# Performance work log

Measured on AMD Instinct MI355X. Metric: run time of the kernel, lower is better.

Reference implementation:

```python
import jax, jax.numpy as jnp
import numpy as np

N, E, B, D, L = 100000, 600000, 128, 128, 3
BOT = 64
EPS = 1e-5


def _forward(query_x, corpus_x, gin_eps, mlp_W1, mlp_b1, mlp_W2, mlp_b2, bn_gamma, bn_beta,
             pool_G1, pool_g1b, pool_G2, pool_g2b, pool_Wm,
             int_G1, int_g1b, int_G2, int_g2b, int_F1, int_f1b, int_F2, int_f2b,
             sc_G1, sc_g1b, sc_G2, sc_g2b, sc_F1, sc_f1b, sc_F2, sc_f2b,
             query_edge_index, query_graph_idx, corpus_edge_index, corpus_graph_idx, num_graphs):
    def gin(x, ei, l):
        # GINConv: sum of source-node features into targets, plus (1+eps)*self
        agg = jax.ops.segment_sum(x[ei[0]], ei[1], num_segments=x.shape[0])
        h = (1.0 + gin_eps[l]) * x + agg
        h = jax.nn.relu(h @ mlp_W1[l] + mlp_b1[l]) @ mlp_W2[l] + mlp_b2[l]
        mu = h.mean(axis=0)
        var = ((h - mu) ** 2).mean(axis=0)  # biased var (BatchNorm training mode)
        h = (h - mu) * jax.lax.rsqrt(var + EPS) * bn_gamma[l] + bn_beta[l]
        return jax.nn.relu(h)  # dropout p=0.0

    def pool(x, gidx, l):
        coef = jnp.tanh(jax.nn.relu(x @ pool_G1[l] + pool_g1b[l]) @ pool_G2[l] + pool_g2b[l])
        s = (coef + 1.0) * x
        sums = jax.ops.segment_sum(s, gidx, num_segments=num_graphs)
        cnt = jax.ops.segment_sum(jnp.ones((x.shape[0],), x.dtype), gidx, num_segments=num_graphs)
        mean = sums / cnt[:, None]
        gc = jnp.tanh(mean @ pool_Wm[l])  # [B, D]
        node_coef = jax.nn.sigmoid(jnp.sum(s * gc[gidx], axis=1))  # [N]
        return jax.ops.segment_sum(node_coef[:, None] * s, gidx, num_segments=num_graphs)

    def interact(q, c, l):
        comb = jnp.concatenate([q, c], axis=1)  # [B, 2D]
        coef = jax.nn.sigmoid(jax.nn.relu(comb @ int_G1[l] + int_g1b[l]) @ int_G2[l] + int_g2b[l])
        sc = (coef + 1.0) * comb
        return jax.nn.relu(jax.nn.relu(sc @ int_F1[l] + int_f1b[l]) @ int_F2[l] + int_f2b[l])

    qx, cx = query_x, corpus_x
    feats = []
    for l in range(gin_eps.shape[0]):
        qx = gin(qx, query_edge_index, l)
        cx = gin(cx, corpus_edge_index, l)
        feats.append(interact(pool(qx, query_graph_idx, l), pool(cx, corpus_graph_idx, l), l))
    f = jnp.concatenate(feats, axis=1)  # [B, sum(filters)//2]
    coef = jax.nn.sigmoid(jax.nn.relu(f @ sc_G1 + sc_g1b) @ sc_G2 + sc_g2b)
    sf = (coef + 1.0) * f
    return (jax.nn.relu(sf @ sc_F1 + sc_f1b) @ sc_F2 + sc_f2b).squeeze(-1)  # [B]


def setup_inputs() -> dict:
    key = jax.random.key(0)
    kit = iter(jax.random.split(key, 64))
    def nrm(shape, s=0.05):
        return jax.random.normal(next(kit), shape, jnp.float32) * s
    C, R, OUT, AGG, RG = 2 * D, (2 * D) // 4, D // 2, (3 * D) // 2, ((3 * D) // 2) // 4
    inp = {
        "query_x": nrm((N, D), 1.0),
        "query_edge_index": jax.random.randint(next(kit), (2, E), 0, N),
        "query_graph_idx": jnp.sort(jax.random.randint(next(kit), (N,), 0, B)),
        "corpus_x": nrm((N, D), 1.0),
        "corpus_edge_index": jax.random.randint(next(kit), (2, E), 0, N),
        "corpus_graph_idx": jnp.sort(jax.random.randint(next(kit), (N,), 0, B)),
        "num_graphs": B,
        "gin_eps": jnp.zeros((L,), jnp.float32),
        "mlp_W1": nrm((L, D, D)), "mlp_b1": jnp.zeros((L, D)),
        "mlp_W2": nrm((L, D, D)), "mlp_b2": jnp.zeros((L, D)),
        "bn_gamma": jnp.ones((L, D)), "bn_beta": jnp.zeros((L, D)),
        "pool_G1": nrm((L, D, D // 4)), "pool_g1b": jnp.zeros((L, D // 4)),
        "pool_G2": nrm((L, D // 4, D)), "pool_g2b": jnp.zeros((L, D)),
        "pool_Wm": nrm((L, D, D)),
        "int_G1": nrm((L, C, R)), "int_g1b": jnp.zeros((L, R)),
        "int_G2": nrm((L, R, C)), "int_g2b": jnp.zeros((L, C)),
        "int_F1": nrm((L, C, C)), "int_f1b": jnp.zeros((L, C)),
        "int_F2": nrm((L, C, OUT)), "int_f2b": jnp.zeros((L, OUT)),
        "sc_G1": nrm((AGG, RG)), "sc_g1b": jnp.zeros((RG,)),
        "sc_G2": nrm((RG, AGG)), "sc_g2b": jnp.zeros((AGG,)),
        "sc_F1": nrm((AGG, BOT)), "sc_f1b": jnp.zeros((BOT,)),
        "sc_F2": nrm((BOT, 1)), "sc_f2b": jnp.zeros((1,)),
    }
    return inp


def reference(query_x, query_edge_index, query_graph_idx, corpus_x, corpus_edge_index, corpus_graph_idx,
              num_graphs, gin_eps, mlp_W1, mlp_b1, mlp_W2, mlp_b2, bn_gamma, bn_beta,
              pool_G1, pool_g1b, pool_G2, pool_g2b, pool_Wm,
              int_G1, int_g1b, int_G2, int_g2b, int_F1, int_f1b, int_F2, int_f2b,
              sc_G1, sc_g1b, sc_G2, sc_g2b, sc_F1, sc_f1b, sc_F2, sc_f2b):
    return _forward(query_x, corpus_x, gin_eps, mlp_W1, mlp_b1, mlp_W2, mlp_b2, bn_gamma, bn_beta,
                    pool_G1, pool_g1b, pool_G2, pool_g2b, pool_Wm,
                    int_G1, int_g1b, int_G2, int_g2b, int_F1, int_f1b, int_F2, int_f2b,
                    sc_G1, sc_g1b, sc_G2, sc_g2b, sc_F1, sc_f1b, sc_F2, sc_f2b,
                    query_edge_index, query_graph_idx, corpus_edge_index, corpus_graph_idx, num_graphs)
```

## Files before the change

### kernel.cpp

```cpp
#include <hip/hip_runtime.h>
#include <hip/hip_bf16.h>

constexpr int NN  = 100000;
constexpr int NN2 = 200000;
constexpr int NE  = 600000;
constexpr int NB  = 128;
constexpr int D   = 128;
constexpr int NL  = 3;
constexpr int CAP = 48;
constexpr int MT_TOT = NN2 / 16;
constexpr int MT_Q   = NN / 16;

typedef __bf16 bf16x8 __attribute__((ext_vector_type(8)));
typedef float f32x4 __attribute__((ext_vector_type(4)));
typedef unsigned short us8 __attribute__((ext_vector_type(8)));

__device__ __forceinline__ float sigmoidf_(float x) { return 1.0f / (1.0f + __expf(-x)); }
__device__ __forceinline__ unsigned short f2b(float f) {
    __hip_bfloat16 h = __float2bfloat16(f);
    return __builtin_bit_cast(unsigned short, h);
}
__device__ __forceinline__ float b2f(unsigned short u) {
    __hip_bfloat16 h = __builtin_bit_cast(__hip_bfloat16, u);
    return __bfloat162float(h);
}
__device__ __forceinline__ bf16x8 ldfrag(const unsigned short* p) {
    return __builtin_bit_cast(bf16x8, *(const us8*)p);
}

__global__ __launch_bounds__(256) void k_csr_fill(const int* __restrict__ qei, const int* __restrict__ cei,
                                                  int* __restrict__ deg, int* __restrict__ bucket) {
    int e = blockIdx.x * 256 + threadIdx.x;
    int src, dst;
    if (e < NE) {
        src = qei[e]; dst = qei[NE + e];
    } else if (e < 2 * NE) {
        src = cei[e - NE] + NN; dst = cei[NE + (e - NE)] + NN;
    } else return;
    int pos = atomicAdd(&deg[dst], 1);
    if (pos < CAP) bucket[(size_t)dst * CAP + pos] = src;
}

__global__ __launch_bounds__(256) void k_cnt(const int* __restrict__ gq, const int* __restrict__ gc,
                                             float* __restrict__ cnt) {
    __shared__ float h[256];
    for (int i = threadIdx.x; i < 256; i += 256) h[i] = 0.f;
    __syncthreads();
    int total = gridDim.x * 256;
    int tid = blockIdx.x * 256 + threadIdx.x;
    int per = (NN2 + total - 1) / total;
    int r0 = tid * per, r1 = min(r0 + per, NN2);
    if (r0 < r1) {
        int cur = (r0 < NN) ? gq[r0] : 128 + gc[r0 - NN];
        float c = 0.f;
        for (int r = r0; r < r1; ++r) {
            int g = (r < NN) ? gq[r] : 128 + gc[r - NN];
            if (g != cur) { atomicAdd(&h[cur], c); c = 0.f; cur = g; }
            c += 1.f;
        }
        atomicAdd(&h[cur], c);
    }
    __syncthreads();
    for (int i = threadIdx.x; i < 256; i += 256)
        if (h[i] != 0.f) atomicAdd(&cnt[i], h[i]);
}

__global__ __launch_bounds__(256) void k_wprep_all(
    const float* mW1, const float* mW2, const float* pG1, const float* pG2,
    const float* iG1, const float* iG2, const float* iF1, const float* iF2,
    const float* sG1, const float* sG2, const float* sF1,
    unsigned short* W1t, unsigned short* W2t, unsigned short* G1t, unsigned short* G2t,
    unsigned short* iG1t, unsigned short* iG2t, unsigned short* iF1t, unsigned short* iF2t,
    unsigned short* sG1t, unsigned short* sG2t, unsigned short* sF1t) {
    int i = blockIdx.x * 256 + threadIdx.x;
#define SEG(CNT, KK, NN_, SRC, DST)                                              \
    if (i < (CNT)) {                                                             \
        int l = i / ((KK) * (NN_)), r = i % ((KK) * (NN_));                      \
        int n = r / (KK), k = r % (KK);                                          \
        DST[i] = f2b(SRC[(size_t)l * (KK) * (NN_) + (size_t)k * (NN_) + n]);     \
        return;                                                                  \
    }                                                                            \
    i -= (CNT);
    SEG(49152, 128, 128, mW1, W1t)
    SEG(49152, 128, 128, mW2, W2t)
    SEG(12288, 128, 32, pG1, G1t)
    SEG(12288, 32, 128, pG2, G2t)
    SEG(49152, 256, 64, iG1, iG1t)
    SEG(49152, 64, 256, iG2, iG2t)
    SEG(196608, 256, 256, iF1, iF1t)
    SEG(49152, 256, 64, iF2, iF2t)
    SEG(9216, 192, 48, sG1, sG1t)
    if (i < 12288) {
        int n = i / 64, k = i % 64;
        sG2t[i] = (k < 48) ? f2b(sG2[(size_t)k * 192 + n]) : (unsigned short)0;
        return;
    }
    i -= 12288;
    SEG(12288, 192, 64, sF1, sF1t)
#undef SEG
}

constexpr int HSTR = 136;
template <bool BF16IN>
__global__ __launch_bounds__(256, 2) void k_gmlp(const float* __restrict__ qx, const float* __restrict__ cx,
                                                 const unsigned short* __restrict__ xb,
                                                 unsigned short* __restrict__ hout,
                                                 const int* __restrict__ deg, const int* __restrict__ bucket,
                                                 const float* __restrict__ eps_p, int l,
                                                 const unsigned short* __restrict__ W1t,
                                                 const unsigned short* __restrict__ W2t,
                                                 const float* __restrict__ b1,
                                                 const float* __restrict__ b2,
                                                 float* __restrict__ stat) {
    __shared__ unsigned short zt[16 * HSTR];
    __shared__ unsigned short ht[16 * HSTR];
    __shared__ float red[512];
    int wave = threadIdx.x >> 6, lane = threadIdx.x & 63;
    int col16 = lane & 15, quad = lane >> 4;
    bf16x8 bf1[2][4], bf2[2][4];
    float bb1[2], bb2[2];
#pragma unroll
    for (int t = 0; t < 2; ++t) {
        int c = wave * 32 + t * 16 + col16;
        bb1[t] = b1[c]; bb2[t] = b2[c];
#pragma unroll
        for (int kc = 0; kc < 4; ++kc) {
            bf1[t][kc] = ldfrag(W1t + (size_t)c * D + kc * 32 + quad * 8);
            bf2[t][kc] = ldfrag(W2t + (size_t)c * D + kc * 32 + quad * 8);
        }
    }
    float e = 1.0f + eps_p[l];
    int gr = threadIdx.x >> 4, c8 = threadIdx.x & 15;
    float cs[2][2] = {{0.f, 0.f}, {0.f, 0.f}};
    float cq[2][2] = {{0.f, 0.f}, {0.f, 0.f}};
    int iters = (MT_TOT + gridDim.x - 1) / gridDim.x;
    for (int n = 0; n < iters; ++n) {
        int mt = blockIdx.x + n * gridDim.x;
        bool act = (mt < MT_TOT);
        int row = (act ? mt : 0) * 16 + gr;
        float a[8];
        const float* base = nullptr; int off = 0;
        if constexpr (BF16IN) {
            us8 v = *(const us8*)(xb + (size_t)row * D + c8 * 8);
#pragma unroll
            for (int j = 0; j < 8; ++j) a[j] = e * b2f(v[j]);
        } else {
            base = (row < NN) ? qx : cx; off = (row < NN) ? 0 : NN;
            float4 v0 = *(const float4*)(base + (size_t)(row - off) * D + c8 * 8);
            float4 v1 = *(const float4*)(base + (size_t)(row - off) * D + c8 * 8 + 4);
            a[0] = e * v0.x; a[1] = e * v0.y; a[2] = e * v0.z; a[3] = e * v0.w;
            a[4] = e * v1.x; a[5] = e * v1.y; a[6] = e * v1.z; a[7] = e * v1.w;
        }
        int d = act ? deg[row] : 0; d = (d < CAP) ? d : CAP;
        const int* bk = bucket + (size_t)row * CAP;
        int i = 0;
        for (; i + 4 <= d; i += 4) {
            int s0 = bk[i], s1 = bk[i + 1], s2 = bk[i + 2], s3 = bk[i + 3];
            if constexpr (BF16IN) {
                us8 u0 = *(const us8*)(xb + (size_t)s0 * D + c8 * 8);
                us8 u1 = *(const us8*)(xb + (size_t)s1 * D + c8 * 8);
                us8 u2 = *(const us8*)(xb + (size_t)s2 * D + c8 * 8);
                us8 u3 = *(const us8*)(xb + (size_t)s3 * D + c8 * 8);
#pragma unroll
                for (int j = 0; j < 8; ++j)
                    a[j] += b2f(u0[j]) + b2f(u1[j]) + b2f(u2[j]) + b2f(u3[j]);
            } else {
                const float* p0 = base + (size_t)(s0 - off) * D + c8 * 8;
                const float* p1 = base + (size_t)(s1 - off) * D + c8 * 8;
                const float* p2 = base + (size_t)(s2 - off) * D + c8 * 8;
                const float* p3 = base + (size_t)(s3 - off) * D + c8 * 8;
                float4 w0 = *(const float4*)p0, w0b = *(const float4*)(p0 + 4);
                float4 w1 = *(const float4*)p1, w1b = *(const float4*)(p1 + 4);
                float4 w2 = *(const float4*)p2, w2b = *(const float4*)(p2 + 4);
                float4 w3 = *(const float4*)p3, w3b = *(const float4*)(p3 + 4);
                a[0] += w0.x + w1.x + w2.x + w3.x; a[1] += w0.y + w1.y + w2.y + w3.y;
                a[2] += w0.z + w1.z + w2.z + w3.z; a[3] += w0.w + w1.w + w2.w + w3.w;
                a[4] += w0b.x + w1b.x + w2b.x + w3b.x; a[5] += w0b.y + w1b.y + w2b.y + w3b.y;
                a[6] += w0b.z + w1b.z + w2b.z + w3b.z; a[7] += w0b.w + w1b.w + w2b.w + w3b.w;
            }
        }
        for (; i < d; ++i) {
            int s0 = bk[i];
            if constexpr (BF16IN) {
                us8 u0 = *(const us8*)(xb + (size_t)s0 * D + c8 * 8);
#pragma unroll
                for (int j = 0; j < 8; ++j) a[j] += b2f(u0[j]);
            } else {
                const float* p0 = base + (size_t)(s0 - off) * D + c8 * 8;
                float4 w0 = *(const float4*)p0, w0b = *(const float4*)(p0 + 4);
                a[0] += w0.x; a[1] += w0.y; a[2] += w0.z; a[3] += w0.w;
                a[4] += w0b.x; a[5] += w0b.y; a[6] += w0b.z; a[7] += w0b.w;
            }
        }
        us8 o;
#pragma unroll
        for (int j = 0; j < 8; ++j) o[j] = f2b(a[j]);
        *(us8*)(zt + gr * HSTR + c8 * 8) = o;
        __syncthreads();
        {
            f32x4 acc[2];
#pragma unroll
            for (int t = 0; t < 2; ++t) acc[t] = (f32x4){0.f, 0.f, 0.f, 0.f};
#pragma unroll
            for (int kc = 0; kc < 4; ++kc) {
                bf16x8 af = ldfrag(zt + col16 * HSTR + kc * 32 + quad * 8);
#pragma unroll
                for (int t = 0; t < 2; ++t)
                    acc[t] = __builtin_amdgcn_mfma_f32_16x16x32_bf16(af, bf1[t][kc], acc[t], 0, 0, 0);
            }
#pragma unroll
            for (int t = 0; t < 2; ++t) {
                int c = wave * 32 + t * 16 + col16;
#pragma unroll
                for (int r = 0; r < 4; ++r)
                    ht[(quad * 4 + r) * HSTR + c] = f2b(fmaxf(acc[t][r] + bb1[t], 0.f));
            }
        }
        __syncthreads();
        {
            f32x4 acc[2];
#pragma unroll
            for (int t = 0; t < 2; ++t) acc[t] = (f32x4){0.f, 0.f, 0.f, 0.f};
#pragma unroll
            for (int kc = 0; kc < 4; ++kc) {
                bf16x8 af = ldfrag(ht + col16 * HSTR + kc * 32 + quad * 8);
#pragma unroll
                for (int t = 0; t < 2; ++t)
                    acc[t] = __builtin_amdgcn_mfma_f32_16x16x32_bf16(af, bf2[t][kc], acc[t], 0, 0, 0);
            }
            if (act) {
                int side = (mt < MT_Q) ? 0 : 1;
#pragma unroll
                for (int t = 0; t < 2; ++t) {
                    int c = wave * 32 + t * 16 + col16;
#pragma unroll
                    for (int r = 0; r < 4; ++r) {
                        int m = mt * 16 + quad * 4 + r;
                        float v = acc[t][r] + bb2[t];
                        hout[(size_t)m * D + c] = f2b(v);
                        cs[side][t] += v; cq[side][t] += v * v;
                    }
                }
            }
        }
    }
    for (int i = threadIdx.x; i < 512; i += 256) red[i] = 0.f;
    __syncthreads();
#pragma unroll
    for (int t = 0; t < 2; ++t) {
        int c = wave * 32 + t * 16 + col16;
#pragma unroll
        for (int side = 0; side < 2; ++side) {
            atomicAdd(&red[side * 256 + c], cs[side][t]);
            atomicAdd(&red[side * 256 + 128 + c], cq[side][t]);
        }
    }
    __syncthreads();
    for (int i = threadIdx.x; i < 512; i += 256) atomicAdd(&stat[i], red[i]);
}

__global__ __launch_bounds__(256, 2) void k_pool(const unsigned short* __restrict__ H,
                                                 const unsigned short* __restrict__ G1t,
                                                 const unsigned short* __restrict__ G2t,
                                                 const float* __restrict__ b1,
                                                 const float* __restrict__ b2,
                                                 const float* __restrict__ stat,
                                                 const float* __restrict__ gamma,
                                                 const float* __restrict__ beta,
                                                 const int* __restrict__ gq, const int* __restrict__ gcix,
                                                 unsigned short* __restrict__ Xo,
                                                 unsigned short* __restrict__ S,
                                                 float* __restrict__ seg_sum) {
    __shared__ float sc_s[256], sh_s[256];
    __shared__ unsigned short xt[4][16 * HSTR];
    __shared__ unsigned short t2t[4][16 * 40];
    {
        int t = threadIdx.x, side = t >> 7, c = t & 127;
        const float invN = 1.0f / (float)NN;
        float mu = stat[side * 256 + c] * invN;
        float var = fmaxf(stat[side * 256 + 128 + c] * invN - mu * mu, 0.f);
        float inv = rsqrtf(var + 1e-5f);
        float s = gamma[c] * inv;
        sc_s[t] = s;
        sh_s[t] = beta[c] - mu * s;
    }
    __syncthreads();
    int wave = threadIdx.x >> 6, lane = threadIdx.x & 63;
    int col16 = lane & 15, quad = lane >> 4;
    unsigned short* xtile = xt[wave];
    unsigned short* t2tile = t2t[wave];
    int nwaves = gridDim.x * 4;
    int per = (MT_TOT + nwaves - 1) / nwaves;
    int wid = blockIdx.x * 4 + wave;
    int mt0 = wid * per, mt1 = min(mt0 + per, MT_TOT);
    if (mt0 >= mt1) return;

    bf16x8 g1f[2][4], g2f[8];
    float bb1[2], bb2[8];
#pragma unroll
    for (int t = 0; t < 2; ++t) {
        int c = t * 16 + col16;
        bb1[t] = b1[c];
#pragma unroll
        for (int kc = 0; kc < 4; ++kc)
            g1f[t][kc] = ldfrag(G1t + (size_t)c * D + kc * 32 + quad * 8);
    }
#pragma unroll
    for (int t = 0; t < 8; ++t) {
        int c = t * 16 + col16;
        bb2[t] = b2[c];
        g2f[t] = ldfrag(G2t + (size_t)c * 32 + quad * 8);
    }
    float sacc[8] = {0.f, 0.f, 0.f, 0.f, 0.f, 0.f, 0.f, 0.f};
    int curg = -1;
    for (int mt = mt0; mt < mt1; ++mt) {
        int side = (mt < MT_Q) ? 0 : 1;
        const float* scp = sc_s + side * 128;
        const float* shp = sh_s + side * 128;
        const unsigned short* Hp = H + ((size_t)mt * 16 + col16) * D + quad * 8;
        unsigned short* Xp = Xo + ((size_t)mt * 16 + col16) * D + quad * 8;
        f32x4 acc1[2];
#pragma unroll
        for (int t = 0; t < 2; ++t) acc1[t] = (f32x4){0.f, 0.f, 0.f, 0.f};
#pragma unroll
        for (int kc = 0; kc < 4; ++kc) {
            us8 hv = *(const us8*)(Hp + kc * 32);
            int k0 = kc * 32 + quad * 8;
            float4 s0 = *(const float4*)&scp[k0], s1 = *(const float4*)&scp[k0 + 4];
            float4 h0 = *(const float4*)&shp[k0], h1 = *(const float4*)&shp[k0 + 4];
            us8 xv;
            xv[0] = f2b(fmaxf(b2f(hv[0]) * s0.x + h0.x, 0.f));
            xv[1] = f2b(fmaxf(b2f(hv[1]) * s0.y + h0.y, 0.f));
            xv[2] = f2b(fmaxf(b2f(hv[2]) * s0.z + h0.z, 0.f));
            xv[3] = f2b(fmaxf(b2f(hv[3]) * s0.w + h0.w, 0.f));
            xv[4] = f2b(fmaxf(b2f(hv[4]) * s1.x + h1.x, 0.f));
            xv[5] = f2b(fmaxf(b2f(hv[5]) * s1.y + h1.y, 0.f));
            xv[6] = f2b(fmaxf(b2f(hv[6]) * s1.z + h1.z, 0.f));
            xv[7] = f2b(fmaxf(b2f(hv[7]) * s1.w + h1.w, 0.f));
            *(us8*)(Xp + kc * 32) = xv;
            *(us8*)(xtile + col16 * HSTR + k0) = xv;
            bf16x8 af = __builtin_bit_cast(bf16x8, xv);
#pragma unroll
            for (int t = 0; t < 2; ++t)
                acc1[t] = __builtin_amdgcn_mfma_f32_16x16x32_bf16(af, g1f[t][kc], acc1[t], 0, 0, 0);
        }
#pragma unroll
        for (int t = 0; t < 2; ++t) {
            int c = t * 16 + col16;
#pragma unroll
            for (int r = 0; r < 4; ++r)
                t2tile[(quad * 4 + r) * 40 + c] = f2b(fmaxf(acc1[t][r] + bb1[t], 0.f));
        }
        bf16x8 af2 = ldfrag(t2tile + col16 * 40 + quad * 8);
        f32x4 acc2[8];
#pragma unroll
        for (int t = 0; t < 8; ++t) {
            acc2[t] = (f32x4){0.f, 0.f, 0.f, 0.f};
            acc2[t] = __builtin_amdgcn_mfma_f32_16x16x32_bf16(af2, g2f[t], acc2[t], 0, 0, 0);
        }
#pragma unroll
        for (int r = 0; r < 4; ++r) {
            int m = mt * 16 + quad * 4 + r;
            int g = (m < NN) ? gq[m] : 128 + gcix[m - NN];
            if (g != curg) {
                if (curg >= 0) {
#pragma unroll
                    for (int t = 0; t < 8; ++t) {
                        atomicAdd(&seg_sum[(size_t)curg * D + t * 16 + col16], sacc[t]);
                        sacc[t] = 0.f;
                    }
                }
                curg = g;
            }
#pragma unroll
            for (int t = 0; t < 8; ++t) {
                int c = t * 16 + col16;
                float v = (tanhf(acc2[t][r] + bb2[t]) + 1.f) * b2f(xtile[(quad * 4 + r) * HSTR + c]);
                S[(size_t)m * D + c] = f2b(v);
                sacc[t] += v;
            }
        }
    }
    if (curg >= 0) {
#pragma unroll
        for (int t = 0; t < 8; ++t)
            atomicAdd(&seg_sum[(size_t)curg * D + t * 16 + col16], sacc[t]);
    }
}

__global__ void k_gc(const float* __restrict__ sums, const float* __restrict__ cnt,
                     const float* __restrict__ Wm, float* __restrict__ gc) {
    __shared__ float m[D];
    int b = blockIdx.x, j = threadIdx.x;
    m[j] = sums[b * D + j] / cnt[b];
    __syncthreads();
    float a = 0.f;
#pragma unroll 8
    for (int i = 0; i < D; ++i) a += m[i] * Wm[i * D + j];
    gc[b * D + j] = tanhf(a);
}

__global__ __launch_bounds__(256) void k_ncseg(const unsigned short* __restrict__ S,
                                               const int* __restrict__ gq, const int* __restrict__ gc,
                                               const float* __restrict__ gcb,
                                               float* __restrict__ dq, float* __restrict__ dc) {
    int stream = blockIdx.x * 4 + (threadIdx.x >> 6);
    int lane = threadIdx.x & 63;
    int nstream = gridDim.x * 4;
    int per = (NN2 + nstream - 1) / nstream;
    int r0 = stream * per;
    int r1 = min(r0 + per, NN2);
    if (r0 >= r1) return;
    float a0 = 0.f, a1 = 0.f;
    int cur = (r0 < NN) ? gq[r0] : 128 + gc[r0 - NN];
    for (int r = r0; r < r1; ++r) {
        int g = (r < NN) ? gq[r] : 128 + gc[r - NN];
        if (g != cur) {
            float* base = (cur < 128) ? (dq + cur * D) : (dc + (cur - 128) * D);
            atomicAdd(&base[lane * 2], a0);
            atomicAdd(&base[lane * 2 + 1], a1);
            a0 = 0.f; a1 = 0.f; cur = g;
        }
        ushort2 sv = *(const ushort2*)&S[(size_t)r * D + lane * 2];
        float2 gv = *(const float2*)&gcb[(size_t)g * D + lane * 2];
        float v0 = b2f(sv.x), v1 = b2f(sv.y);
        float p = v0 * gv.x + v1 * gv.y;
#pragma unroll
        for (int off = 1; off < 64; off <<= 1) p += __shfl_xor(p, off, 64);
        float nc = sigmoidf_(p);
        a0 += nc * v0; a1 += nc * v1;
    }
    float* base = (cur < 128) ? (dq + cur * D) : (dc + (cur - 128) * D);
    atomicAdd(&base[lane * 2], a0);
    atomicAdd(&base[lane * 2 + 1], a1);
}

constexpr int LSTR = 264;
__global__ __launch_bounds__(256) void k_interact(const float* __restrict__ pooled,
                                                  const unsigned short* __restrict__ iG1t, const float* __restrict__ ig1b,
                                                  const unsigned short* __restrict__ iG2t, const float* __restrict__ ig2b,
                                                  const unsigned short* __restrict__ iF1t, const float* __restrict__ if1b,
                                                  const unsigned short* __restrict__ iF2t, const float* __restrict__ if2b,
                                                  unsigned short* __restrict__ featsb) {
    __shared__ unsigned short bufC[16 * LSTR];
    __shared__ unsigned short bufA[16 * LSTR];
    __shared__ unsigned short bufB[16 * LSTR];
    int t = threadIdx.x, wave = t >> 6, lane = t & 63;
    int col16 = lane & 15, quad = lane >> 4;
    int pg = blockIdx.x & 7, l = blockIdx.x >> 3;
    int p0 = pg * 16;
    {
        int r = t >> 4, c0 = (t & 15) * 16;
        const float* src = (c0 < 128)
            ? (pooled + (size_t)l * NB * D + (size_t)(p0 + r) * D + c0)
            : (pooled + (size_t)(NL + l) * NB * D + (size_t)(p0 + r) * D + (c0 - 128));
#pragma unroll
        for (int j = 0; j < 16; ++j) bufC[r * LSTR + c0 + j] = f2b(src[j]);
    }
    __syncthreads();
    {
        f32x4 acc = (f32x4){0.f, 0.f, 0.f, 0.f};
        int n = wave * 16 + col16;
#pragma unroll
        for (int kc = 0; kc < 8; ++kc) {
            bf16x8 af = ldfrag(&bufC[col16 * LSTR + kc * 32 + quad * 8]);
            bf16x8 bfr = ldfrag(iG1t + ((size_t)l * 64 + n) * 256 + kc * 32 + quad * 8);
            acc = __builtin_amdgcn_mfma_f32_16x16x32_bf16(af, bfr, acc, 0, 0, 0);
        }
        float bb = ig1b[(size_t)l * 64 + n];
#pragma unroll
        for (int r = 0; r < 4; ++r)
            bufA[(quad * 4 + r) * LSTR + n] = f2b(fmaxf(acc[r] + bb, 0.f));
    }
    __syncthreads();
    {
        f32x4 acc[4];
#pragma unroll
        for (int tt = 0; tt < 4; ++tt) acc[tt] = (f32x4){0.f, 0.f, 0.f, 0.f};
#pragma unroll
        for (int kc = 0; kc < 2; ++kc) {
            bf16x8 af = ldfrag(&bufA[col16 * LSTR + kc * 32 + quad * 8]);
#pragma unroll
            for (int tt = 0; tt < 4; ++tt) {
                int n = wave * 64 + tt * 16 + col16;
                bf16x8 bfr = ldfrag(iG2t + ((size_t)l * 256 + n) * 64 + kc * 32 + quad * 8);
                acc[tt] = __builtin_amdgcn_mfma_f32_16x16x32_bf16(af, bfr, acc[tt], 0, 0, 0);
            }
        }
#pragma unroll
        for (int tt = 0; tt < 4; ++tt) {
            int n = wave * 64 + tt * 16 + col16;
            float bb = ig2b[(size_t)l * 256 + n];
#pragma unroll
            for (int r = 0; r < 4; ++r) {
                int row = quad * 4 + r;
                float s = (sigmoidf_(acc[tt][r] + bb) + 1.f) * b2f(bufC[row * LSTR + n]);
                bufB[row * LSTR + n] = f2b(s);
            }
        }
    }
    __syncthreads();
    {
        f32x4 acc[4];
#pragma unroll
        for (int tt = 0; tt < 4; ++tt) acc[tt] = (f32x4){0.f, 0.f, 0.f, 0.f};
#pragma unroll
        for (int kc = 0; kc < 8; ++kc) {
            bf16x8 af = ldfrag(&bufB[col16 * LSTR + kc * 32 + quad * 8]);
#pragma unroll
            for (int tt = 0; tt < 4; ++tt) {
                int n = wave * 64 + tt * 16 + col16;
                bf16x8 bfr = ldfrag(iF1t + (size_t)l * 256 * 256 + (size_t)n * 256 + kc * 32 + quad * 8);
                acc[tt] = __builtin_amdgcn_mfma_f32_16x16x32_bf16(af, bfr, acc[tt], 0, 0, 0);
            }
        }
#pragma unroll
        for (int tt = 0; tt < 4; ++tt) {
            int n = wave * 64 + tt * 16 + col16;
            float bb = if1b[(size_t)l * 256 + n];
#pragma unroll
            for (int r = 0; r < 4; ++r)
                bufA[(quad * 4 + r) * LSTR + n] = f2b(fmaxf(acc[tt][r] + bb, 0.f));
        }
    }
    __syncthreads();
    {
        f32x4 acc = (f32x4){0.f, 0.f, 0.f, 0.f};
        int n = wave * 16 + col16;
#pragma unroll
        for (int kc = 0; kc < 8; ++kc) {
            bf16x8 af = ldfrag(&bufA[col16 * LSTR + kc * 32 + quad * 8]);
            bf16x8 bfr = ldfrag(iF2t + ((size_t)l * 64 + n) * 256 + kc * 32 + quad * 8);
            acc = __builtin_amdgcn_mfma_f32_16x16x32_bf16(af, bfr, acc, 0, 0, 0);
        }
        float bb = if2b[(size_t)l * 64 + n];
#pragma unroll
        for (int r = 0; r < 4; ++r)
            featsb[(size_t)(p0 + quad * 4 + r) * 192 + l * 64 + n] = f2b(fmaxf(acc[r] + bb, 0.f));
    }
}

__global__ __launch_bounds__(256) void k_score(const unsigned short* __restrict__ featsb,
                                               const unsigned short* __restrict__ sG1t, const float* __restrict__ sg1b,
                                               const unsigned short* __restrict__ sG2t, const float* __restrict__ sg2b,
                                               const unsigned short* __restrict__ sF1t, const float* __restrict__ sf1b,
                                               const float* __restrict__ sF2, const float* __restrict__ sf2b,
                                               float* __restrict__ out) {
    __shared__ unsigned short bufF[16 * 200];
    __shared__ unsigned short bufA[16 * LSTR];
    __shared__ unsigned short bufB[16 * LSTR];
    __shared__ float redf[16 * 65];
    int t = threadIdx.x, wave = t >> 6, lane = t & 63;
    int col16 = lane & 15, quad = lane >> 4;
    int p0 = blockIdx.x * 16;
    {
        int r = t >> 4, c0 = (t & 15) * 12;
#pragma unroll
        for (int j = 0; j < 12; ++j)
            bufF[r * 200 + c0 + j] = featsb[(size_t)(p0 + r) * 192 + c0 + j];
    }
    __syncthreads();
    if (wave < 3) {
        f32x4 acc = (f32x4){0.f, 0.f, 0.f, 0.f};
        int n = wave * 16 + col16;
#pragma unroll
        for (int kc = 0; kc < 6; ++kc) {
            bf16x8 af = ldfrag(&bufF[col16 * 200 + kc * 32 + quad * 8]);
            bf16x8 bfr = ldfrag(sG1t + (size_t)n * 192 + kc * 32 + quad * 8);
            acc = __builtin_amdgcn_mfma_f32_16x16x32_bf16(af, bfr, acc, 0, 0, 0);
        }
        float bb = sg1b[n];
#pragma unroll
        for (int r = 0; r < 4; ++r)
            bufA[(quad * 4 + r) * LSTR + n] = f2b(fmaxf(acc[r] + bb, 0.f));
    } else {
        int row = lane >> 2, c = 48 + (lane & 3) * 4;
#pragma unroll
        for (int j = 0; j < 4; ++j) bufA[row * LSTR + c + j] = 0;
    }
    __syncthreads();
    {
        f32x4 acc[3];
#pragma unroll
        for (int tt = 0; tt < 3; ++tt) acc[tt] = (f32x4){0.f, 0.f, 0.f, 0.f};
#pragma unroll
        for (int kc = 0; kc < 2; ++kc) {
            bf16x8 af = ldfrag(&bufA[col16 * LSTR + kc * 32 + quad * 8]);
#pragma unroll
            for (int tt = 0; tt < 3; ++tt) {
                int n = wave * 48 + tt * 16 + col16;
                bf16x8 bfr = ldfrag(sG2t + (size_t)n * 64 + kc * 32 + quad * 8);
                acc[tt] = __builtin_amdgcn_mfma_f32_16x16x32_bf16(af, bfr, acc[tt], 0, 0, 0);
            }
        }
#pragma unroll
        for (int tt = 0; tt < 3; ++tt) {
            int n = wave * 48 + tt * 16 + col16;
            float bb = sg2b[n];
#pragma unroll
            for (int r = 0; r < 4; ++r) {
                int row = quad * 4 + r;
                float s = (sigmoidf_(acc[tt][r] + bb) + 1.f) * b2f(bufF[row * 200 + n]);
                bufB[row * LSTR + n] = f2b(s);
            }
        }
    }
    __syncthreads();
    {
        f32x4 acc = (f32x4){0.f, 0.f, 0.f, 0.f};
        int n = wave * 16 + col16;
#pragma unroll
        for (int kc = 0; kc < 6; ++kc) {
            bf16x8 af = ldfrag(&bufB[col16 * LSTR + kc * 32 + quad * 8]);
            bf16x8 bfr = ldfrag(sF1t + (size_t)n * 192 + kc * 32 + quad * 8);
            acc = __builtin_amdgcn_mfma_f32_16x16x32_bf16(af, bfr, acc, 0, 0, 0);
        }
        float bb = sf1b[n], w2 = sF2[n];
#pragma unroll
        for (int r = 0; r < 4; ++r)
            redf[(quad * 4 + r) * 65 + n] = fmaxf(acc[r] + bb, 0.f) * w2;
    }
    __syncthreads();
    if (t < 16) {
        float s = 0.f;
#pragma unroll 8
        for (int i = 0; i < 64; ++i) s += redf[t * 65 + i];
        out[p0 + t] = s + sf2b[0];
    }
}

extern "C" void kernel_launch(void* const* d_in, const int* in_sizes, int n_in,
                              void* d_out, int out_size, void* d_ws, size_t ws_size,
                              hipStream_t stream) {
    const float* query_x   = (const float*)d_in[0];
    const int*   query_ei  = (const int*)d_in[1];
    const int*   query_gi  = (const int*)d_in[2];
    const float* corpus_x  = (const float*)d_in[3];
    const int*   corpus_ei = (const int*)d_in[4];
    const int*   corpus_gi = (const int*)d_in[5];
    const float* gin_eps   = (const float*)d_in[7];
    const float* mlp_W1    = (const float*)d_in[8];
    const float* mlp_b1    = (const float*)d_in[9];
    const float* mlp_W2    = (const float*)d_in[10];
    const float* mlp_b2    = (const float*)d_in[11];
    const float* bn_gamma  = (const float*)d_in[12];
    const float* bn_beta   = (const float*)d_in[13];
    const float* pool_G1   = (const float*)d_in[14];
    const float* pool_g1b  = (const float*)d_in[15];
    const float* pool_G2   = (const float*)d_in[16];
    const float* pool_g2b  = (const float*)d_in[17];
    const float* pool_Wm   = (const float*)d_in[18];
    const float* int_G1    = (const float*)d_in[19];
    const float* int_g1b   = (const float*)d_in[20];
    const float* int_G2    = (const float*)d_in[21];
    const float* int_g2b   = (const float*)d_in[22];
    const float* int_F1    = (const float*)d_in[23];
    const float* int_f1b   = (const float*)d_in[24];
    const float* int_F2    = (const float*)d_in[25];
    const float* int_f2b   = (const float*)d_in[26];
    const float* sc_G1     = (const float*)d_in[27];
    const float* sc_g1b    = (const float*)d_in[28];
    const float* sc_G2     = (const float*)d_in[29];
    const float* sc_g2b    = (const float*)d_in[30];
    const float* sc_F1     = (const float*)d_in[31];
    const float* sc_f1b    = (const float*)d_in[32];
    const float* sc_F2     = (const float*)d_in[33];
    const float* sc_f2b    = (const float*)d_in[34];
    float* out = (float*)d_out;

    unsigned short* Zb  = (unsigned short*)d_ws;
    unsigned short* Xb  = Zb + (size_t)NN2 * D;
    unsigned short* Sb  = Xb + (size_t)NN2 * D;
    unsigned short* featsb = Sb + (size_t)NN2 * D;
    unsigned short* W1t = featsb + 128 * 192;
    unsigned short* W2t = W1t + NL * D * D;
    unsigned short* G1t = W2t + NL * D * D;
    unsigned short* G2t = G1t + NL * 32 * D;
    unsigned short* iG1t = G2t + NL * D * 32;
    unsigned short* iG2t = iG1t + NL * 64 * 256;
    unsigned short* iF1t = iG2t + NL * 256 * 64;
    unsigned short* iF2t = iF1t + NL * 256 * 256;
    unsigned short* sG1t = iF2t + NL * 64 * 256;
    unsigned short* sG2t = sG1t + 48 * 192;
    unsigned short* sF1t = sG2t + 192 * 64;
    int* deg    = (int*)(sF1t + 64 * 192);
    int* bucket = deg + NN2;
    float* bn_stat  = (float*)(bucket + (size_t)NN2 * CAP);
    float* seg_sum  = bn_stat + NL * 512;
    float* seg_cnt  = seg_sum + 256 * D;
    float* gcb      = seg_cnt + 256;
    float* pooled   = gcb + 256 * D;

    k_wprep_all<<<1956, 256, 0, stream>>>(mlp_W1, mlp_W2, pool_G1, pool_G2,
                                          int_G1, int_G2, int_F1, int_F2,
                                          sc_G1, sc_G2, sc_F1,
                                          W1t, W2t, G1t, G2t, iG1t, iG2t, iF1t, iF2t,
                                          sG1t, sG2t, sF1t);

    hipMemsetAsync(deg, 0, NN2 * sizeof(int), stream);
    hipMemsetAsync(bn_stat, 0, NL * 512 * sizeof(float), stream);
    hipMemsetAsync(pooled, 0, 2 * NL * NB * D * sizeof(float), stream);
    hipMemsetAsync(seg_cnt, 0, 256 * sizeof(float), stream);
    k_csr_fill<<<(2 * NE + 255) / 256, 256, 0, stream>>>(query_ei, corpus_ei, deg, bucket);
    k_cnt<<<64, 256, 0, stream>>>(query_gi, corpus_gi, seg_cnt);

    for (int l = 0; l < NL; ++l) {
        if (l == 0)
            k_gmlp<false><<<1024, 256, 0, stream>>>(query_x, corpus_x, nullptr, Zb,
                                                    deg, bucket, gin_eps, l,
                                                    W1t + (size_t)l * D * D, W2t + (size_t)l * D * D,
                                                    mlp_b1 + l * D, mlp_b2 + l * D, bn_stat + l * 512);
        else
            k_gmlp<true><<<1024, 256, 0, stream>>>(nullptr, nullptr, Xb, Zb,
                                                   deg, bucket, gin_eps, l,
                                                   W1t + (size_t)l * D * D, W2t + (size_t)l * D * D,
                                                   mlp_b1 + l * D, mlp_b2 + l * D, bn_stat + l * 512);
        hipMemsetAsync(seg_sum, 0, 256 * D * sizeof(float), stream);
        k_pool<<<782, 256, 0, stream>>>(Zb, G1t + (size_t)l * 32 * D, G2t + (size_t)l * D * 32,
                                        pool_g1b + l * 32, pool_g2b + l * D,
                                        bn_stat + l * 512, bn_gamma + l * D, bn_beta + l * D,
                                        query_gi, corpus_gi, Xb, Sb, seg_sum);
        k_gc<<<256, D, 0, stream>>>(seg_sum, seg_cnt, pool_Wm + (size_t)l * D * D, gcb);
        k_ncseg<<<1024, 256, 0, stream>>>(Sb, query_gi, corpus_gi, gcb,
                                          pooled + (size_t)l * NB * D,
                                          pooled + (size_t)(NL + l) * NB * D);
    }
    k_interact<<<24, 256, 0, stream>>>(pooled, iG1t, int_g1b, iG2t, int_g2b,
                                       iF1t, int_f1b, iF2t, int_f2b, featsb);
    k_score<<<8, 256, 0, stream>>>(featsb, sG1t, sc_g1b, sG2t, sc_g2b,
                                   sF1t, sc_f1b, sc_F2, sc_f2b, out);
}
```

Before: 1.117 ms.

## Restructure GIN MLP kernel: one 32-row tile per block, padded neighbor buckets

The persistent grid-stride GIN aggregation+MLP kernel becomes a one-tile-per-block kernel that handles 32 rows. It no longer keeps the weight fragments in registers; it reloads them per tile from global memory, and the launch bound rises to allow 6 blocks per CU. Neighbor buckets are padded to a multiple of 8 with a sentinel index that points at a zeroed extra row of the bf16 features. This lets layers 1-2 gather 8 neighbors per step with vectorized index loads and no tail loop. The aim is more memory-level parallelism on the irregular gather, at the cost of an extra pad kernel, repeated weight loads and more per-block atomics into the BN statistics.

```diff
diff --git a/kernel.cpp b/kernel.cpp
--- a/kernel.cpp
+++ b/kernel.cpp
@@ -10,6 +10,7 @@
 constexpr int CAP = 48;
 constexpr int MT_TOT = NN2 / 16;
 constexpr int MT_Q   = NN / 16;
+constexpr int ST_TOT = MT_TOT / 2;
 
 typedef __bf16 bf16x8 __attribute__((ext_vector_type(8)));
 typedef float f32x4 __attribute__((ext_vector_type(4)));
@@ -39,6 +40,14 @@
     } else return;
     int pos = atomicAdd(&deg[dst], 1);
     if (pos < CAP) bucket[(size_t)dst * CAP + pos] = src;
+}
+
+__global__ __launch_bounds__(256) void k_pad(const int* __restrict__ deg, int* __restrict__ bucket) {
+    int r = blockIdx.x * 256 + threadIdx.x;
+    if (r >= NN2) return;
+    int d = deg[r]; d = (d < CAP) ? d : CAP;
+    int dp = (d + 7) & ~7; dp = (dp < CAP) ? dp : CAP;
+    for (int i = d; i < dp; ++i) bucket[(size_t)r * CAP + i] = NN2;
 }
 
 __global__ __launch_bounds__(256) void k_cnt(const int* __restrict__ gq, const int* __restrict__ gc,
@@ -102,7 +111,7 @@
 
 constexpr int HSTR = 136;
 template <bool BF16IN>
-__global__ __launch_bounds__(256, 2) void k_gmlp(const float* __restrict__ qx, const float* __restrict__ cx,
+__global__ __launch_bounds__(256, 6) void k_gmlp(const float* __restrict__ qx, const float* __restrict__ cx,
                                                  const unsigned short* __restrict__ xb,
                                                  unsigned short* __restrict__ hout,
                                                  const int* __restrict__ deg, const int* __restrict__ bucket,
@@ -112,151 +121,157 @@
                                                  const float* __restrict__ b1,
                                                  const float* __restrict__ b2,
                                                  float* __restrict__ stat) {
-    __shared__ unsigned short zt[16 * HSTR];
-    __shared__ unsigned short ht[16 * HSTR];
-    __shared__ float red[512];
-    int wave = threadIdx.x >> 6, lane = threadIdx.x & 63;
+    __shared__ unsigned short zt[32 * HSTR];
+    __shared__ unsigned short ht[32 * HSTR];
+    __shared__ float red[256];
+    int tid = threadIdx.x;
+    red[tid] = 0.f;
+    int base = blockIdx.x * 32;
+    int wave = tid >> 6, lane = tid & 63;
     int col16 = lane & 15, quad = lane >> 4;
-    bf16x8 bf1[2][4], bf2[2][4];
-    float bb1[2], bb2[2];
+    int gr = tid >> 4, c8 = tid & 15;
+    float e = 1.0f + eps_p[l];
 #pragma unroll
     for (int t = 0; t < 2; ++t) {
-        int c = wave * 32 + t * 16 + col16;
-        bb1[t] = b1[c]; bb2[t] = b2[c];
-#pragma unroll
-        for (int kc = 0; kc < 4; ++kc) {
-            bf1[t][kc] = ldfrag(W1t + (size_t)c * D + kc * 32 + quad * 8);
-            bf2[t][kc] = ldfrag(W2t + (size_t)c * D + kc * 32 + quad * 8);
-        }
-    }
-    float e = 1.0f + eps_p[l];
-    int gr = threadIdx.x >> 4, c8 = threadIdx.x & 15;
-    float cs[2][2] = {{0.f, 0.f}, {0.f, 0.f}};
-    float cq[2][2] = {{0.f, 0.f}, {0.f, 0.f}};
-    int iters = (MT_TOT + gridDim.x - 1) / gridDim.x;
-    for (int n = 0; n < iters; ++n) {
-        int mt = blockIdx.x + n * gridDim.x;
-        bool act = (mt < MT_TOT);
-        int row = (act ? mt : 0) * 16 + gr;
+        int row = base + t * 16 + gr;
         float a[8];
-        const float* base = nullptr; int off = 0;
         if constexpr (BF16IN) {
             us8 v = *(const us8*)(xb + (size_t)row * D + c8 * 8);
 #pragma unroll
             for (int j = 0; j < 8; ++j) a[j] = e * b2f(v[j]);
+            int d = deg[row]; d = (d < CAP) ? d : CAP;
+            int dp = (d + 7) & ~7; dp = (dp < CAP) ? dp : CAP;
+            const int* bk = bucket + (size_t)row * CAP;
+            for (int i = 0; i < dp; i += 8) {
+                int4 bi0 = *(const int4*)(bk + i);
+                int4 bi1 = *(const int4*)(bk + i + 4);
+                us8 u0 = *(const us8*)(xb + (size_t)bi0.x * D + c8 * 8);
+                us8 u1 = *(const us8*)(xb + (size_t)bi0.y * D + c8 * 8);
+                us8 u2 = *(const us8*)(xb + (size_t)bi0.z * D + c8 * 8);
+                us8 u3 = *(const us8*)(xb + (size_t)bi0.w * D + c8 * 8);
+                us8 u4 = *(const us8*)(xb + (size_t)bi1.x * D + c8 * 8);
+                us8 u5 = *(const us8*)(xb + (size_t)bi1.y * D + c8 * 8);
+                us8 u6 = *(const us8*)(xb + (size_t)bi1.z * D + c8 * 8);
+                us8 u7 = *(const us8*)(xb + (size_t)bi1.w * D + c8 * 8);
+#pragma unroll
+                for (int j = 0; j < 8; ++j)
+                    a[j] += b2f(u0[j]) + b2f(u1[j]) + b2f(u2[j]) + b2f(u3[j])
+                          + b2f(u4[j]) + b2f(u5[j]) + b2f(u6[j]) + b2f(u7[j]);
+            }
         } else {
-            base = (row < NN) ? qx : cx; off = (row < NN) ? 0 : NN;
-            float4 v0 = *(const float4*)(base + (size_t)(row - off) * D + c8 * 8);
-            float4 v1 = *(const float4*)(base + (size_t)(row - off) * D + c8 * 8 + 4);
+            const float* bs = (row < NN) ? qx : cx;
+            int off = (row < NN) ? 0 : NN;
+            const float* sp = bs + (size_t)(row - off) * D + c8 * 8;
+            float4 v0 = *(const float4*)sp;
+            float4 v1 = *(const float4*)(sp + 4);
             a[0] = e * v0.x; a[1] = e * v0.y; a[2] = e * v0.z; a[3] = e * v0.w;
             a[4] = e * v1.x; a[5] = e * v1.y; a[6] = e * v1.z; a[7] = e * v1.w;
-        }
-        int d = act ? deg[row] : 0; d = (d < CAP) ? d : CAP;
-        const int* bk = bucket + (size_t)row * CAP;
-        int i = 0;
-        for (; i + 4 <= d; i += 4) {
-            int s0 = bk[i], s1 = bk[i + 1], s2 = bk[i + 2], s3 = bk[i + 3];
-            if constexpr (BF16IN) {
-                us8 u0 = *(const us8*)(xb + (size_t)s0 * D + c8 * 8);
-                us8 u1 = *(const us8*)(xb + (size_t)s1 * D + c8 * 8);
-                us8 u2 = *(const us8*)(xb + (size_t)s2 * D + c8 * 8);
-                us8 u3 = *(const us8*)(xb + (size_t)s3 * D + c8 * 8);
-#pragma unroll
-                for (int j = 0; j < 8; ++j)
-                    a[j] += b2f(u0[j]) + b2f(u1[j]) + b2f(u2[j]) + b2f(u3[j]);
-            } else {
-                const float* p0 = base + (size_t)(s0 - off) * D + c8 * 8;
-                const float* p1 = base + (size_t)(s1 - off) * D + c8 * 8;
-                const float* p2 = base + (size_t)(s2 - off) * D + c8 * 8;
-                const float* p3 = base + (size_t)(s3 - off) * D + c8 * 8;
+            int d = deg[row]; d = (d < CAP) ? d : CAP;
+            int dp = (d + 3) & ~3;
+            const int* bk = bucket + (size_t)row * CAP;
+            for (int i = 0; i < dp; i += 4) {
+                int4 bi = *(const int4*)(bk + i);
+                int s0 = (i + 0 < d) ? bi.x : row;
+                int s1 = (i + 1 < d) ? bi.y : row;
+                int s2 = (i + 2 < d) ? bi.z : row;
+                int s3 = (i + 3 < d) ? bi.w : row;
+                float m0 = (i + 0 < d) ? 1.f : 0.f;
+                float m1 = (i + 1 < d) ? 1.f : 0.f;
+                float m2 = (i + 2 < d) ? 1.f : 0.f;
+                float m3 = (i + 3 < d) ? 1.f : 0.f;
+                const float* p0 = bs + (size_t)(s0 - off) * D + c8 * 8;
+                const float* p1 = bs + (size_t)(s1 - off) * D + c8 * 8;
+                const float* p2 = bs + (size_t)(s2 - off) * D + c8 * 8;
+                const float* p3 = bs + (size_t)(s3 - off) * D + c8 * 8;
                 float4 w0 = *(const float4*)p0, w0b = *(const float4*)(p0 + 4);
                 float4 w1 = *(const float4*)p1, w1b = *(const float4*)(p1 + 4);
                 float4 w2 = *(const float4*)p2, w2b = *(const float4*)(p2 + 4);
                 float4 w3 = *(const float4*)p3, w3b = *(const float4*)(p3 + 4);
-                a[0] += w0.x + w1.x + w2.x + w3.x; a[1] += w0.y + w1.y + w2.y + w3.y;
-                a[2] += w0.z + w1.z + w2.z + w3.z; a[3] += w0.w + w1.w + w2.w + w3.w;
-                a[4] += w0b.x + w1b.x + w2b.x + w3b.x; a[5] += w0b.y + w1b.y + w2b.y + w3b.y;
-                a[6] += w0b.z + w1b.z + w2b.z + w3b.z; a[7] += w0b.w + w1b.w + w2b.w + w3b.w;
-            }
-        }
-        for (; i < d; ++i) {
-            int s0 = bk[i];
-            if constexpr (BF16IN) {
-                us8 u0 = *(const us8*)(xb + (size_t)s0 * D + c8 * 8);
-#pragma unroll
-                for (int j = 0; j < 8; ++j) a[j] += b2f(u0[j]);
-            } else {
-                const float* p0 = base + (size_t)(s0 - off) * D + c8 * 8;
-                float4 w0 = *(const float4*)p0, w0b = *(const float4*)(p0 + 4);
-                a[0] += w0.x; a[1] += w0.y; a[2] += w0.z; a[3] += w0.w;
-                a[4] += w0b.x; a[5] += w0b.y; a[6] += w0b.z; a[7] += w0b.w;
+                a[0] += m0 * w0.x + m1 * w1.x + m2 * w2.x + m3 * w3.x;
+                a[1] += m0 * w0.y + m1 * w1.y + m2 * w2.y + m3 * w3.y;
+                a[2] += m0 * w0.z + m1 * w1.z + m2 * w2.z + m3 * w3.z;
+                a[3] += m0 * w0.w + m1 * w1.w + m2 * w2.w + m3 * w3.w;
+                a[4] += m0 * w0b.x + m1 * w1b.x + m2 * w2b.x + m3 * w3b.x;
+                a[5] += m0 * w0b.y + m1 * w1b.y + m2 * w2b.y + m3 * w3b.y;
+                a[6] += m0 * w0b.z + m1 * w1b.z + m2 * w2b.z + m3 * w3b.z;
+                a[7] += m0 * w0b.w + m1 * w1b.w + m2 * w2b.w + m3 * w3b.w;
             }
         }
         us8 o;
 #pragma unroll
         for (int j = 0; j < 8; ++j) o[j] = f2b(a[j]);
-        *(us8*)(zt + gr * HSTR + c8 * 8) = o;
+        *(us8*)(zt + (t * 16 + gr) * HSTR + c8 * 8) = o;
+    }
+    __syncthreads();
+    {
+        f32x4 acc[2][2];
+#pragma unroll
+        for (int t2 = 0; t2 < 2; ++t2)
+#pragma unroll
+            for (int ct = 0; ct < 2; ++ct) acc[t2][ct] = (f32x4){0.f, 0.f, 0.f, 0.f};
+#pragma unroll
+        for (int kc = 0; kc < 4; ++kc) {
+            bf16x8 af0 = ldfrag(zt + col16 * HSTR + kc * 32 + quad * 8);
+            bf16x8 af1 = ldfrag(zt + (16 + col16) * HSTR + kc * 32 + quad * 8);
+#pragma unroll
+            for (int ct = 0; ct < 2; ++ct) {
+                int c = wave * 32 + ct * 16 + col16;
+                bf16x8 wf = ldfrag(W1t + (size_t)c * D + kc * 32 + quad * 8);
+                acc[0][ct] = __builtin_amdgcn_mfma_f32_16x16x32_bf16(af0, wf, acc[0][ct], 0, 0, 0);
+                acc[1][ct] = __builtin_amdgcn_mfma_f32_16x16x32_bf16(af1, wf, acc[1][ct], 0, 0, 0);
+            }
+        }
+#pragma unroll
+        for (int ct = 0; ct < 2; ++ct) {
+            int c = wave * 32 + ct * 16 + col16;
+            float bb = b1[c];
+#pragma unroll
+            for (int t2 = 0; t2 < 2; ++t2)
+#pragma unroll
+                for (int r = 0; r < 4; ++r)
+                    ht[(t2 * 16 + quad * 4 + r) * HSTR + c] = f2b(fmaxf(acc[t2][ct][r] + bb, 0.f));
+        }
+    }
+    __syncthreads();
+    {
+        f32x4 acc[2][2];
+#pragma unroll
+        for (int t2 = 0; t2 < 2; ++t2)
+#pragma unroll
+            for (int ct = 0; ct < 2; ++ct) acc[t2][ct] = (f32x4){0.f, 0.f, 0.f, 0.f};
+#pragma unroll
+        for (int kc = 0; kc < 4; ++kc) {
+            bf16x8 af0 = ldfrag(ht + col16 * HSTR + kc * 32 + quad * 8);
+            bf16x8 af1 = ldfrag(ht + (16 + col16) * HSTR + kc * 32 + quad * 8);
+#pragma unroll
+            for (int ct = 0; ct < 2; ++ct) {
+                int c = wave * 32 + ct * 16 + col16;
+                bf16x8 wf = ldfrag(W2t + (size_t)c * D + kc * 32 + quad * 8);
+                acc[0][ct] = __builtin_amdgcn_mfma_f32_16x16x32_bf16(af0, wf, acc[0][ct], 0, 0, 0);
+                acc[1][ct] = __builtin_amdgcn_mfma_f32_16x16x32_bf16(af1, wf, acc[1][ct], 0, 0, 0);
+            }
+        }
+        int side = (base < NN) ? 0 : 1;
+#pragma unroll
+        for (int ct = 0; ct < 2; ++ct) {
+            int c = wave * 32 + ct * 16 + col16;
+            float bb = b2[c];
+            float ssum = 0.f, ssq = 0.f;
+#pragma unroll
+            for (int t2 = 0; t2 < 2; ++t2)
+#pragma unroll
+                for (int r = 0; r < 4; ++r) {
+                    int m = base + t2 * 16 + quad * 4 + r;
+                    float v = acc[t2][ct][r] + bb;
+                    hout[(size_t)m * D + c] = f2b(v);
+                    ssum += v; ssq += v * v;
+                }
+            atomicAdd(&red[c], ssum);
+            atomicAdd(&red[128 + c], ssq);
+        }
         __syncthreads();
-        {
-            f32x4 acc[2];
-#pragma unroll
-            for (int t = 0; t < 2; ++t) acc[t] = (f32x4){0.f, 0.f, 0.f, 0.f};
-#pragma unroll
-            for (int kc = 0; kc < 4; ++kc) {
-                bf16x8 af = ldfrag(zt + col16 * HSTR + kc * 32 + quad * 8);
-#pragma unroll
-                for (int t = 0; t < 2; ++t)
-                    acc[t] = __builtin_amdgcn_mfma_f32_16x16x32_bf16(af, bf1[t][kc], acc[t], 0, 0, 0);
-            }
-#pragma unroll
-            for (int t = 0; t < 2; ++t) {
-                int c = wave * 32 + t * 16 + col16;
-#pragma unroll
-                for (int r = 0; r < 4; ++r)
-                    ht[(quad * 4 + r) * HSTR + c] = f2b(fmaxf(acc[t][r] + bb1[t], 0.f));
-            }
-        }
-        __syncthreads();
-        {
-            f32x4 acc[2];
-#pragma unroll
-            for (int t = 0; t < 2; ++t) acc[t] = (f32x4){0.f, 0.f, 0.f, 0.f};
-#pragma unroll
-            for (int kc = 0; kc < 4; ++kc) {
-                bf16x8 af = ldfrag(ht + col16 * HSTR + kc * 32 + quad * 8);
-#pragma unroll
-                for (int t = 0; t < 2; ++t)
-                    acc[t] = __builtin_amdgcn_mfma_f32_16x16x32_bf16(af, bf2[t][kc], acc[t], 0, 0, 0);
-            }
-            if (act) {
-                int side = (mt < MT_Q) ? 0 : 1;
-#pragma unroll
-                for (int t = 0; t < 2; ++t) {
-                    int c = wave * 32 + t * 16 + col16;
-#pragma unroll
-                    for (int r = 0; r < 4; ++r) {
-                        int m = mt * 16 + quad * 4 + r;
-                        float v = acc[t][r] + bb2[t];
-                        hout[(size_t)m * D + c] = f2b(v);
-                        cs[side][t] += v; cq[side][t] += v * v;
-                    }
-                }
-            }
-        }
-    }
-    for (int i = threadIdx.x; i < 512; i += 256) red[i] = 0.f;
-    __syncthreads();
-#pragma unroll
-    for (int t = 0; t < 2; ++t) {
-        int c = wave * 32 + t * 16 + col16;
-#pragma unroll
-        for (int side = 0; side < 2; ++side) {
-            atomicAdd(&red[side * 256 + c], cs[side][t]);
-            atomicAdd(&red[side * 256 + 128 + c], cq[side][t]);
-        }
-    }
-    __syncthreads();
-    for (int i = threadIdx.x; i < 512; i += 256) atomicAdd(&stat[i], red[i]);
+        atomicAdd(&stat[side * 256 + tid], red[tid]);
+    }
 }
 
 __global__ __launch_bounds__(256, 2) void k_pool(const unsigned short* __restrict__ H,
@@ -670,7 +685,7 @@
 
     unsigned short* Zb  = (unsigned short*)d_ws;
     unsigned short* Xb  = Zb + (size_t)NN2 * D;
-    unsigned short* Sb  = Xb + (size_t)NN2 * D;
+    unsigned short* Sb  = Xb + (size_t)(NN2 + 1) * D;
     unsigned short* featsb = Sb + (size_t)NN2 * D;
     unsigned short* W1t = featsb + 128 * 192;
     unsigned short* W2t = W1t + NL * D * D;
@@ -701,20 +716,22 @@
     hipMemsetAsync(bn_stat, 0, NL * 512 * sizeof(float), stream);
     hipMemsetAsync(pooled, 0, 2 * NL * NB * D * sizeof(float), stream);
     hipMemsetAsync(seg_cnt, 0, 256 * sizeof(float), stream);
+    hipMemsetAsync(Xb + (size_t)NN2 * D, 0, D * sizeof(unsigned short), stream);
     k_csr_fill<<<(2 * NE + 255) / 256, 256, 0, stream>>>(query_ei, corpus_ei, deg, bucket);
+    k_pad<<<(NN2 + 255) / 256, 256, 0, stream>>>(deg, bucket);
     k_cnt<<<64, 256, 0, stream>>>(query_gi, corpus_gi, seg_cnt);
 
     for (int l = 0; l < NL; ++l) {
         if (l == 0)
-            k_gmlp<false><<<1024, 256, 0, stream>>>(query_x, corpus_x, nullptr, Zb,
-                                                    deg, bucket, gin_eps, l,
-                                                    W1t + (size_t)l * D * D, W2t + (size_t)l * D * D,
-                                                    mlp_b1 + l * D, mlp_b2 + l * D, bn_stat + l * 512);
+            k_gmlp<false><<<ST_TOT, 256, 0, stream>>>(query_x, corpus_x, nullptr, Zb,
+                                                      deg, bucket, gin_eps, l,
+                                                      W1t + (size_t)l * D * D, W2t + (size_t)l * D * D,
+                                                      mlp_b1 + l * D, mlp_b2 + l * D, bn_stat + l * 512);
         else
-            k_gmlp<true><<<1024, 256, 0, stream>>>(nullptr, nullptr, Xb, Zb,
-                                                   deg, bucket, gin_eps, l,
-                                                   W1t + (size_t)l * D * D, W2t + (size_t)l * D * D,
-                                                   mlp_b1 + l * D, mlp_b2 + l * D, bn_stat + l * 512);
+            k_gmlp<true><<<ST_TOT, 256, 0, stream>>>(nullptr, nullptr, Xb, Zb,
+                                                     deg, bucket, gin_eps, l,
+                                                     W1t + (size_t)l * D * D, W2t + (size_t)l * D * D,
+                                                     mlp_b1 + l * D, mlp_b2 + l * D, bn_stat + l * 512);
         hipMemsetAsync(seg_sum, 0, 256 * D * sizeof(float), stream);
         k_pool<<<782, 256, 0, stream>>>(Zb, G1t + (size_t)l * 32 * D, G2t + (size_t)l * D * 32,
                                         pool_g1b + l * 32, pool_g2b + l * D,
```

After: 1.195 ms. 6.9% more time.
